# Performance work log

Measured on AMD Instinct MI355X. Metric: run time of the kernel, lower is better.

## Reference

```python
import jax, jax.numpy as jnp
import numpy as np
from jax import lax

Q = 16384      # num questions (hyperedges)
S = 16384      # num students (nodes)
F = 64         # feat_dim
EMB = 64       # emb_dim
H = 32         # student_hist_max
C = 16384      # student_attn_chunk_size
E = 393216     # incidence edges per channel (24 chunks)


def setup_inputs() -> dict:
    key = jax.random.key(0)
    ks = jax.random.split(key, 24)
    rn = lambda k, sh, s=1.0: jax.random.normal(k, sh, dtype=jnp.float32) * s
    ri = lambda k, sh, hi: jax.random.randint(k, sh, 0, hi, dtype=jnp.int32)
    return {
        'x': rn(ks[0], (Q, F)),
        's_emb': rn(ks[1], (S, F)),
        'W_Q': rn(ks[2], (2 * F, F), 0.05), 'b_Q': jnp.zeros((F,), jnp.float32),
        'W_K': rn(ks[3], (F, F), 0.05),     'b_K': jnp.zeros((F,), jnp.float32),
        'W_V': rn(ks[4], (F, F), 0.05),     'b_V': jnp.zeros((F,), jnp.float32),
        'W_fuse': rn(ks[5], (2 * F, F), 0.05), 'b_fuse': jnp.zeros((F,), jnp.float32),
        'W_K2': rn(ks[6], (F, F), 0.05),    'b_K2': jnp.zeros((F,), jnp.float32),
        'W_V2': rn(ks[7], (F, F), 0.05),    'b_V2': jnp.zeros((F,), jnp.float32),
        'W_proj': rn(ks[8], (2 * F, EMB), 0.05), 'b_proj': jnp.zeros((EMB,), jnp.float32),
        'h1_bias': jnp.zeros((2, F), jnp.float32),  # nn.init.zeros_ in source
        'h2_bias': jnp.zeros((2, F), jnp.float32),
        'hist_qid_pos': ri(ks[9], (S, H), Q),
        'hist_cnt_pos': ri(ks[10], (S,), H + 1),
        'hist_qid_neg': ri(ks[11], (S, H), Q),
        'hist_cnt_neg': ri(ks[12], (S,), H + 1),
        'edge_sid_pos': ri(ks[13], (E,), S),
        'edge_qid_pos': ri(ks[14], (E,), Q),
        'edge_sid_neg': ri(ks[15], (E,), S),
        'edge_qid_neg': ri(ks[16], (E,), Q),
    }


def reference(x, s_emb, W_Q, b_Q, W_K, b_K, W_V, b_V, W_fuse, b_fuse,
              W_K2, b_K2, W_V2, b_V2, W_proj, b_proj, h1_bias, h2_bias,
              hist_qid_pos, hist_cnt_pos, hist_qid_neg, hist_cnt_neg,
              edge_sid_pos, edge_qid_pos, edge_sid_neg, edge_qid_neg):
    scale = jnp.float32(1.0 / np.sqrt(F))
    NEG = jnp.float32(-1e9)

    def channel(hist_qid, hist_cnt, e_sid, e_qid, ch):
        # dense per-student history keys/values: [S, H, F]
        xh = x[hist_qid]
        Kh = xh @ W_K + b_K + h1_bias[ch]
        Vh = xh @ W_V + b_V
        mask = jnp.arange(H, dtype=jnp.int32)[None, :] < hist_cnt[:, None]  # [S,H]

        def chunk_fn(args):
            sid, qid = args  # [C]
            # edge-level query: W_Q([x_q || e_u])
            q = jnp.concatenate([x[qid], s_emb[sid]], axis=-1) @ W_Q + b_Q  # [C,F]
            sc = jnp.einsum('cf,chf->ch', q, Kh[sid]) * scale               # [C,H]
            m = mask[sid]
            a = jax.nn.softmax(jnp.where(m, sc, NEG), axis=-1)
            a = jnp.where(m, a, 0.0)  # empty history -> zero output
            return jnp.einsum('ch,chf->cf', a, Vh[sid])                     # [C,F]

        nchunks = E // C
        agg = lax.map(chunk_fn, (e_sid.reshape(nchunks, C), e_qid.reshape(nchunks, C)))
        agg = agg.reshape(E, F)
        # fuse student embedding with history-aggregated context
        s_repr = jnp.concatenate([s_emb[e_sid], agg], axis=-1) @ W_fuse + b_fuse  # [E,F]
        # hop 2: question attends over its member students (segment softmax over e_qid)
        k2 = s_repr @ W_K2 + b_K2 + h2_bias[ch]
        v2 = s_repr @ W_V2 + b_V2
        sc2 = jnp.sum(x[e_qid] * k2, axis=-1) * scale                      # [E]
        mx = jax.ops.segment_max(sc2, e_qid, num_segments=Q)
        ex = jnp.exp(sc2 - mx[e_qid])
        den = jax.ops.segment_sum(ex, e_qid, num_segments=Q)
        alpha = ex / jnp.maximum(den[e_qid], 1e-9)
        return jax.ops.segment_sum(alpha[:, None] * v2, e_qid, num_segments=Q)  # [Q,F]

    pos = channel(hist_qid_pos, hist_cnt_pos, edge_sid_pos, edge_qid_pos, 0)
    neg = channel(hist_qid_neg, hist_cnt_neg, edge_sid_neg, edge_qid_neg, 1)
    return jnp.concatenate([pos, neg], axis=-1) @ W_proj + b_proj  # [Q, EMB]
```

## Files before the change

### kernel.cpp

```cpp
#include <hip/hip_runtime.h>

typedef float v2f __attribute__((ext_vector_type(2)));
typedef float v4f __attribute__((ext_vector_type(4)));

#define QN 16384
#define SN 16384
#define HN 32
#define EN 393216
#define KPAD 68

__global__ __launch_bounds__(256) void prep_kernel(
    const float* __restrict__ x, const float* __restrict__ s_emb,
    const float* __restrict__ W_Q, const float* __restrict__ b_Q,
    const float* __restrict__ W_K, const float* __restrict__ b_K,
    const float* __restrict__ W_V, const float* __restrict__ b_V,
    const float* __restrict__ W_fuse, const float* __restrict__ b_fuse,
    const float* __restrict__ W_K2, const float* __restrict__ b_K2,
    const float* __restrict__ h1b, const float* __restrict__ h2b,
    const int* __restrict__ es_pos, const int* __restrict__ es_neg,
    float* __restrict__ xKpos, float* __restrict__ xKneg,
    float* __restrict__ xVfp, float* __restrict__ xQ1, float* __restrict__ xq2p,
    float* __restrict__ c2pos, float* __restrict__ c2neg,
    float* __restrict__ sQ, float* __restrict__ sfp,
    int* __restrict__ cnt_pos, int* __restrict__ cnt_neg)
{
  __shared__ float xs[512];
  __shared__ float vs[512];
  __shared__ float wk2t[64 * 66];
  const int bid = blockIdx.x;
  const int t = threadIdx.x;
  const int j = t & 31, r = t >> 5;

  if (bid < 2048) {
    const int q = bid * 8 + r;
    if (t < 128) *(v4f*)&xs[t * 4] = *(const v4f*)&x[bid * 512 + t * 4];
    for (int i = 0; i < 16; i++) {
      int idx = i * 256 + t;
      wk2t[(idx & 63) * 66 + (idx >> 6)] = W_K2[idx];
    }
    __syncthreads();

    v2f accK = *(const v2f*)&b_K[2 * j];
    v2f accV = *(const v2f*)&b_V[2 * j];
    v2f accQ = {0.f, 0.f};
    float a2x = 0.f, a2y = 0.f;
    for (int g = 0; g < 64; g++) {
      float xv = xs[r * 64 + g];
      accK += xv * *(const v2f*)&W_K[g * 64 + 2 * j];
      accV += xv * *(const v2f*)&W_V[g * 64 + 2 * j];
      accQ += xv * *(const v2f*)&W_Q[g * 64 + 2 * j];
      a2x += xv * wk2t[g * 66 + j];
      a2y += xv * wk2t[g * 66 + j + 32];
    }
    *(v2f*)&xKpos[q * 64 + 2 * j] = accK + *(const v2f*)&h1b[2 * j];
    *(v2f*)&xKneg[q * 64 + 2 * j] = accK + *(const v2f*)&h1b[64 + 2 * j];
    *(v2f*)&xQ1[q * 64 + 2 * j] = accQ;
    v2f a2 = {a2x, a2y};
    *(v2f*)&xq2p[q * 64 + 2 * j] = a2;
    *(v2f*)&vs[r * 64 + 2 * j] = accV;

    v2f xv2 = *(const v2f*)&xs[r * 64 + 2 * j];
    v2f bb0 = *(const v2f*)&b_K2[2 * j] + *(const v2f*)&h2b[2 * j];
    v2f bb1 = *(const v2f*)&b_K2[2 * j] + *(const v2f*)&h2b[64 + 2 * j];
    v2f t0 = xv2 * bb0, t1 = xv2 * bb1;
    float p0 = t0.x + t0.y, p1v = t1.x + t1.y;
    for (int k = 16; k >= 1; k >>= 1) {
      p0 += __shfl_xor(p0, k, 32);
      p1v += __shfl_xor(p1v, k, 32);
    }
    if (j == 0) { c2pos[q] = p0 * 0.125f; c2neg[q] = p1v * 0.125f; }

    __syncthreads();
    float vfx = 0.f, vfy = 0.f;
    for (int g = 0; g < 64; g++) {
      float vv = vs[r * 64 + g];
      vfx += vv * W_fuse[(64 + g) * 64 + j];
      vfy += vv * W_fuse[(64 + g) * 64 + j + 32];
    }
    v2f vf = {vfx, vfy};
    *(v2f*)&xVfp[q * 64 + 2 * j] = vf;
  } else if (bid < 4096) {
    const int b2 = bid - 2048;
    const int s = b2 * 8 + r;
    if (t < 128) *(v4f*)&xs[t * 4] = *(const v4f*)&s_emb[b2 * 512 + t * 4];
    __syncthreads();
    v2f aq = *(const v2f*)&b_Q[2 * j];
    float afx = b_fuse[j], afy = b_fuse[j + 32];
    for (int g = 0; g < 64; g++) {
      float v = xs[r * 64 + g];
      aq += v * *(const v2f*)&W_Q[(64 + g) * 64 + 2 * j];
      afx += v * W_fuse[g * 64 + j];
      afy += v * W_fuse[g * 64 + j + 32];
    }
    *(v2f*)&sQ[s * 64 + 2 * j] = aq;
    v2f af = {afx, afy};
    *(v2f*)&sfp[s * 64 + 2 * j] = af;
  } else {
    const int hb = bid - 4096;
    const bool neg = hb >= 1536;
    const int* __restrict__ sid = neg ? es_neg : es_pos;
    int* __restrict__ cnt = neg ? cnt_neg : cnt_pos;
    const int i = (neg ? hb - 1536 : hb) * 256 + t;
    atomicAdd(&cnt[sid[i]], 1);
  }
}

__global__ __launch_bounds__(256) void scan_kernel(
    const int* __restrict__ cnt_pos, int* __restrict__ beg_pos, int* __restrict__ cur_pos,
    const int* __restrict__ cnt_neg, int* __restrict__ beg_neg, int* __restrict__ cur_neg) {
  const int* cnt = blockIdx.y ? cnt_neg : cnt_pos;
  int* beg = blockIdx.y ? beg_neg : beg_pos;
  int* cur = blockIdx.y ? cur_neg : cur_pos;
  __shared__ int part[256];
  int t = threadIdx.x;
  int s = 0;
  for (int i = 0; i < 64; i++) s += cnt[i * 256 + t];
  part[t] = s;
  __syncthreads();
  for (int off = 1; off < 256; off <<= 1) {
    int v = (t >= off) ? part[t - off] : 0;
    __syncthreads();
    part[t] += v;
    __syncthreads();
  }
  int run = part[t] - s;
  for (int i = 0; i < 64; i++) {
    int id = i * 256 + t;
    int c = cnt[id];
    beg[id] = run; cur[id] = run;
    run += c;
  }
}

__global__ __launch_bounds__(256) void scatter_kernel(
    const int* __restrict__ sid_pos, const int* __restrict__ qid_pos,
    int* __restrict__ cur_pos, int* __restrict__ csr_pos,
    const int* __restrict__ sid_neg, const int* __restrict__ qid_neg,
    int* __restrict__ cur_neg, int* __restrict__ csr_neg, int n) {
  const int* sid = blockIdx.y ? sid_neg : sid_pos;
  const int* qid = blockIdx.y ? qid_neg : qid_pos;
  int* cursor = blockIdx.y ? cur_neg : cur_pos;
  int* csr_qid = blockIdx.y ? csr_neg : csr_pos;
  int i = blockIdx.x * 256 + threadIdx.x;
  if (i < n) {
    int p = atomicAdd(&cursor[sid[i]], 1);
    csr_qid[p] = qid[i];
  }
}

#define LDBATCH(BASE, Q0,Q1,Q2,Q3, A0,A1,A2,A3, X0,X1,X2,X3, C0,C1,C2,C3) do { \
    int _m = ne - 1; \
    Q0 = csr[ebeg + (BASE)]; \
    Q1 = csr[ebeg + min((BASE) + 1, _m)]; \
    Q2 = csr[ebeg + min((BASE) + 2, _m)]; \
    Q3 = csr[ebeg + min((BASE) + 3, _m)]; \
    A0 = *(const v2f*)&xQ1[(size_t)Q0 * 64 + 2 * c] + sqv; \
    A1 = *(const v2f*)&xQ1[(size_t)Q1 * 64 + 2 * c] + sqv; \
    A2 = *(const v2f*)&xQ1[(size_t)Q2 * 64 + 2 * c] + sqv; \
    A3 = *(const v2f*)&xQ1[(size_t)Q3 * 64 + 2 * c] + sqv; \
    X0 = *(const v2f*)&xq2p[(size_t)Q0 * 64 + 2 * c]; \
    X1 = *(const v2f*)&xq2p[(size_t)Q1 * 64 + 2 * c]; \
    X2 = *(const v2f*)&xq2p[(size_t)Q2 * 64 + 2 * c]; \
    X3 = *(const v2f*)&xq2p[(size_t)Q3 * 64 + 2 * c]; \
    C0 = c2[Q0]; C1 = c2[Q1]; C2 = c2[Q2]; C3 = c2[Q3]; \
  } while (0)

__global__ __launch_bounds__(256, 5) void main_kernel(
    const float* __restrict__ xKpos, const float* __restrict__ xKneg,
    const float* __restrict__ xVfp, const float* __restrict__ xQ1,
    const float* __restrict__ xq2p,
    const float* __restrict__ c2pos, const float* __restrict__ c2neg,
    const float* __restrict__ sQ, const float* __restrict__ sfp,
    const int* __restrict__ hq_pos, const int* __restrict__ hc_pos,
    const int* __restrict__ hq_neg, const int* __restrict__ hc_neg,
    const int* __restrict__ beg_pos, const int* __restrict__ cntS_pos,
    const int* __restrict__ csr_pos,
    const int* __restrict__ beg_neg, const int* __restrict__ cntS_neg,
    const int* __restrict__ csr_neg,
    float* __restrict__ num_pos, float* __restrict__ den_pos,
    float* __restrict__ num_neg, float* __restrict__ den_neg)
{
  const int s = blockIdx.x;
  const int ch = blockIdx.y;
  const float* __restrict__ xK = ch ? xKneg : xKpos;
  const float* __restrict__ c2 = ch ? c2neg : c2pos;
  const int* __restrict__ hq = ch ? hq_neg : hq_pos;
  const int* __restrict__ hc = ch ? hc_neg : hc_pos;
  const int* __restrict__ beg = ch ? beg_neg : beg_pos;
  const int* __restrict__ cntS = ch ? cntS_neg : cntS_pos;
  const int* __restrict__ csr = ch ? csr_neg : csr_pos;
  float* __restrict__ num = ch ? num_neg : num_pos;
  float* __restrict__ den = ch ? den_neg : den_pos;

  const int t = threadIdx.x;
  __shared__ float Kl[HN * KPAD];
  __shared__ float Vl[HN * 64];
  __shared__ float Qg[8 * 4 * 64];
  __shared__ float Al[8 * 32 * 4];
  __shared__ int hql[HN];

  const int hcnt = hc[s];
  if (t < HN) hql[t] = hq[s * HN + t];
  __syncthreads();
  for (int i = 0; i < 2; i++) {
    int idx = i * 256 + t;
    int h = idx >> 4, jj = idx & 15;
    int row = hql[h];
    *(v4f*)&Kl[h * KPAD + jj * 4] = *(const v4f*)&xK[(size_t)row * 64 + jj * 4];
    *(v4f*)&Vl[h * 64 + jj * 4] = *(const v4f*)&xVfp[(size_t)row * 64 + jj * 4];
  }
  const int ebeg = beg[s];
  const int ne = cntS[s];
  __syncthreads();

  const float scale = 0.125f;
  const int g = t >> 5;
  const int c = t & 31;
  float* __restrict__ Qb = &Qg[g * 256];
  float* __restrict__ Ab = &Al[g * 128];
  const v4f* kp = (const v4f*)&Kl[c * KPAD];
  const v2f sqv = *(const v2f*)&sQ[(size_t)s * 64 + 2 * c];
  const v2f sfv = *(const v2f*)&sfp[(size_t)s * 64 + 2 * c];

  int i0 = g * 4;
  if (i0 < ne) {
    int q0, q1, q2, q3;
    v2f a0, a1, a2, a3, x20, x21, x22, x23;
    float cc0, cc1, cc2, cc3;
    LDBATCH(i0, q0, q1, q2, q3, a0, a1, a2, a3, x20, x21, x22, x23, cc0, cc1, cc2, cc3);

    for (; i0 < ne; i0 += 32) {
      const int nb = ne - i0;
      *(v2f*)&Qb[2 * c] = a0;
      *(v2f*)&Qb[64 + 2 * c] = a1;
      *(v2f*)&Qb[128 + 2 * c] = a2;
      *(v2f*)&Qb[192 + 2 * c] = a3;

      int n0, n1, n2, n3;
      v2f na0, na1, na2, na3, nx0, nx1, nx2, nx3;
      float nc0, nc1, nc2, nc3;
      const bool more = (i0 + 32) < ne;
      if (more) {
        LDBATCH(i0 + 32, n0, n1, n2, n3, na0, na1, na2, na3,
                nx0, nx1, nx2, nx3, nc0, nc1, nc2, nc3);
      }

      float s0 = 0.f, s1 = 0.f, s2 = 0.f, s3 = 0.f;
#pragma unroll 4
      for (int k = 0; k < 16; k++) {
        v4f k4 = kp[k];
        v4f qa = ((const v4f*)&Qb[0])[k];
        s0 += qa.x * k4.x + qa.y * k4.y + qa.z * k4.z + qa.w * k4.w;
        v4f qb = ((const v4f*)&Qb[64])[k];
        s1 += qb.x * k4.x + qb.y * k4.y + qb.z * k4.z + qb.w * k4.w;
        v4f qc = ((const v4f*)&Qb[128])[k];
        s2 += qc.x * k4.x + qc.y * k4.y + qc.z * k4.z + qc.w * k4.w;
        v4f qd = ((const v4f*)&Qb[192])[k];
        s3 += qd.x * k4.x + qd.y * k4.y + qd.z * k4.z + qd.w * k4.w;
      }
      const bool valid = (c < hcnt);
      float e0 = valid ? __expf(s0 * scale) : 0.f;
      float e1 = valid ? __expf(s1 * scale) : 0.f;
      float e2 = valid ? __expf(s2 * scale) : 0.f;
      float e3 = valid ? __expf(s3 * scale) : 0.f;
      float d0 = e0, d1 = e1, d2 = e2, d3 = e3;
      for (int k = 16; k >= 1; k >>= 1) {
        d0 += __shfl_xor(d0, k, 32);
        d1 += __shfl_xor(d1, k, 32);
        d2 += __shfl_xor(d2, k, 32);
        d3 += __shfl_xor(d3, k, 32);
      }
      v4f av;
      av.x = (d0 > 0.f) ? e0 / d0 : 0.f;
      av.y = (d1 > 0.f) ? e1 / d1 : 0.f;
      av.z = (d2 > 0.f) ? e2 / d2 : 0.f;
      av.w = (d3 > 0.f) ? e3 / d3 : 0.f;
      *(v4f*)&Ab[c * 4] = av;

      v2f r0 = sfv, r1 = sfv, r2 = sfv, r3 = sfv;
#pragma unroll 8
      for (int h = 0; h < HN; h++) {
        v2f vv = *(const v2f*)&Vl[h * 64 + 2 * c];
        v4f a4 = *(const v4f*)&Ab[h * 4];
        r0 += a4.x * vv;
        r1 += a4.y * vv;
        r2 += a4.z * vv;
        r3 += a4.w * vv;
      }

      {
        float p = r0.x * x20.x + r0.y * x20.y;
        for (int k = 16; k >= 1; k >>= 1) p += __shfl_xor(p, k, 32);
        float ew = __expf(p * scale + cc0);
        atomicAdd(&num[(size_t)q0 * 64 + c], ew * r0.x);
        atomicAdd(&num[(size_t)q0 * 64 + 32 + c], ew * r0.y);
        if (c == 0) atomicAdd(&den[q0], ew);
      }
      if (nb > 1) {
        float p = r1.x * x21.x + r1.y * x21.y;
        for (int k = 16; k >= 1; k >>= 1) p += __shfl_xor(p, k, 32);
        float ew = __expf(p * scale + cc1);
        atomicAdd(&num[(size_t)q1 * 64 + c], ew * r1.x);
        atomicAdd(&num[(size_t)q1 * 64 + 32 + c], ew * r1.y);
        if (c == 0) atomicAdd(&den[q1], ew);
      }
      if (nb > 2) {
        float p = r2.x * x22.x + r2.y * x22.y;
        for (int k = 16; k >= 1; k >>= 1) p += __shfl_xor(p, k, 32);
        float ew = __expf(p * scale + cc2);
        atomicAdd(&num[(size_t)q2 * 64 + c], ew * r2.x);
        atomicAdd(&num[(size_t)q2 * 64 + 32 + c], ew * r2.y);
        if (c == 0) atomicAdd(&den[q2], ew);
      }
      if (nb > 3) {
        float p = r3.x * x23.x + r3.y * x23.y;
        for (int k = 16; k >= 1; k >>= 1) p += __shfl_xor(p, k, 32);
        float ew = __expf(p * scale + cc3);
        atomicAdd(&num[(size_t)q3 * 64 + c], ew * r3.x);
        atomicAdd(&num[(size_t)q3 * 64 + 32 + c], ew * r3.y);
        if (c == 0) atomicAdd(&den[q3], ew);
      }

      q0 = n0; q1 = n1; q2 = n2; q3 = n3;
      a0 = na0; a1 = na1; a2 = na2; a3 = na3;
      x20 = nx0; x21 = nx1; x22 = nx2; x23 = nx3;
      cc0 = nc0; cc1 = nc1; cc2 = nc2; cc3 = nc3;
    }
  }
}

__global__ __launch_bounds__(256) void final_kernel(
    const float* __restrict__ num_pos, const float* __restrict__ den_pos,
    const float* __restrict__ num_neg, const float* __restrict__ den_neg,
    const float* __restrict__ W_V2, const float* __restrict__ b_V2,
    const float* __restrict__ W_proj, const float* __restrict__ b_proj,
    float* __restrict__ out)
{
  __shared__ float np[8 * 64], nn[8 * 64], hp[8 * 64], hn[8 * 64];
  int t = threadIdx.x;
  int j = t & 31, r = t >> 5;
  int q = blockIdx.x * 8 + r;
  if (t < 128) {
    *(v4f*)&np[t * 4] = *(const v4f*)&num_pos[blockIdx.x * 512 + t * 4];
    *(v4f*)&nn[t * 4] = *(const v4f*)&num_neg[blockIdx.x * 512 + t * 4];
  }
  __syncthreads();
  float dp = den_pos[q], dn = den_neg[q];
  float ip = (dp > 0.f) ? 1.f / dp : 0.f;
  float in_ = (dn > 0.f) ? 1.f / dn : 0.f;
  v2f zero = {0.f, 0.f};
  v2f bv = *(const v2f*)&b_V2[2 * j];
  v2f hpv = (dp > 0.f) ? bv : zero;
  v2f hnv = (dn > 0.f) ? bv : zero;
  for (int f = 0; f < 64; f++) {
    v2f w = *(const v2f*)&W_V2[f * 64 + 2 * j];
    hpv += (np[r * 64 + f] * ip) * w;
    hnv += (nn[r * 64 + f] * in_) * w;
  }
  *(v2f*)&hp[r * 64 + 2 * j] = hpv;
  *(v2f*)&hn[r * 64 + 2 * j] = hnv;
  __syncthreads();
  v2f o = *(const v2f*)&b_proj[2 * j];
  for (int f = 0; f < 64; f++) {
    o += hp[r * 64 + f] * *(const v2f*)&W_proj[f * 64 + 2 * j];
    o += hn[r * 64 + f] * *(const v2f*)&W_proj[(64 + f) * 64 + 2 * j];
  }
  *(v2f*)&out[q * 64 + 2 * j] = o;
}

extern "C" void kernel_launch(void* const* d_in, const int* in_sizes, int n_in,
                              void* d_out, int out_size, void* d_ws, size_t ws_size,
                              hipStream_t stream) {
  const float* x      = (const float*)d_in[0];
  const float* s_emb  = (const float*)d_in[1];
  const float* W_Q    = (const float*)d_in[2];
  const float* b_Q    = (const float*)d_in[3];
  const float* W_K    = (const float*)d_in[4];
  const float* b_K    = (const float*)d_in[5];
  const float* W_V    = (const float*)d_in[6];
  const float* b_V    = (const float*)d_in[7];
  const float* W_fuse = (const float*)d_in[8];
  const float* b_fuse = (const float*)d_in[9];
  const float* W_K2   = (const float*)d_in[10];
  const float* b_K2   = (const float*)d_in[11];
  const float* W_V2   = (const float*)d_in[12];
  const float* b_V2   = (const float*)d_in[13];
  const float* W_proj = (const float*)d_in[14];
  const float* b_proj = (const float*)d_in[15];
  const float* h1b    = (const float*)d_in[16];
  const float* h2b    = (const float*)d_in[17];
  const int* hq_pos   = (const int*)d_in[18];
  const int* hc_pos   = (const int*)d_in[19];
  const int* hq_neg   = (const int*)d_in[20];
  const int* hc_neg   = (const int*)d_in[21];
  const int* es_pos   = (const int*)d_in[22];
  const int* eq_pos   = (const int*)d_in[23];
  const int* es_neg   = (const int*)d_in[24];
  const int* eq_neg   = (const int*)d_in[25];
  float* out = (float*)d_out;

  size_t off = 0;
  char* base = (char*)d_ws;
  auto carve = [&](size_t bytes) -> void* {
    void* p = base + off;
    off += (bytes + 255) & ~(size_t)255;
    return p;
  };
  float* num_pos = (float*)carve((size_t)QN * 64 * 4);
  float* num_neg = (float*)carve((size_t)QN * 64 * 4);
  float* den_pos = (float*)carve((size_t)QN * 4);
  float* den_neg = (float*)carve((size_t)QN * 4);
  int* cnt_pos   = (int*)carve((size_t)SN * 4);
  int* cnt_neg   = (int*)carve((size_t)SN * 4);
  size_t zero_bytes = off;
  float* xKpos = (float*)carve((size_t)QN * 64 * 4);
  float* xKneg = (float*)carve((size_t)QN * 64 * 4);
  float* xVfp  = (float*)carve((size_t)QN * 64 * 4);
  float* xQ1   = (float*)carve((size_t)QN * 64 * 4);
  float* xq2p  = (float*)carve((size_t)QN * 64 * 4);
  float* sQ    = (float*)carve((size_t)SN * 64 * 4);
  float* sfp   = (float*)carve((size_t)SN * 64 * 4);
  float* c2pos = (float*)carve((size_t)QN * 4);
  float* c2neg = (float*)carve((size_t)QN * 4);
  int* beg_pos = (int*)carve((size_t)SN * 4);
  int* beg_neg = (int*)carve((size_t)SN * 4);
  int* cur_pos = (int*)carve((size_t)SN * 4);
  int* cur_neg = (int*)carve((size_t)SN * 4);
  int* csr_pos = (int*)carve((size_t)EN * 4);
  int* csr_neg = (int*)carve((size_t)EN * 4);
  if (off > ws_size) return;

  hipMemsetAsync(d_ws, 0, zero_bytes, stream);

  prep_kernel<<<4096 + 2 * (EN / 256), 256, 0, stream>>>(
      x, s_emb, W_Q, b_Q, W_K, b_K, W_V, b_V, W_fuse, b_fuse, W_K2, b_K2,
      h1b, h2b, es_pos, es_neg,
      xKpos, xKneg, xVfp, xQ1, xq2p, c2pos, c2neg, sQ, sfp,
      cnt_pos, cnt_neg);

  scan_kernel<<<dim3(1, 2), 256, 0, stream>>>(cnt_pos, beg_pos, cur_pos,
                                              cnt_neg, beg_neg, cur_neg);
  scatter_kernel<<<dim3(EN / 256, 2), 256, 0, stream>>>(es_pos, eq_pos, cur_pos, csr_pos,
                                                        es_neg, eq_neg, cur_neg, csr_neg, EN);

  main_kernel<<<dim3(SN, 2), 256, 0, stream>>>(
      xKpos, xKneg, xVfp, xQ1, xq2p, c2pos, c2neg, sQ, sfp,
      hq_pos, hc_pos, hq_neg, hc_neg,
      beg_pos, cnt_pos, csr_pos, beg_neg, cnt_neg, csr_neg,
      num_pos, den_pos, num_neg, den_neg);

  final_kernel<<<QN / 8, 256, 0, stream>>>(num_pos, den_pos, num_neg, den_neg,
                                           W_V2, b_V2, W_proj, b_proj, out);
}
```

Measured before the change: 602.4 us.

## Replace hop-2 atomic scatter with question-sorted edge buffer and segment reduction

```diff
diff --git a/kernel.cpp b/kernel.cpp
--- a/kernel.cpp
+++ b/kernel.cpp
@@ -8,6 +8,7 @@
 #define HN 32
 #define EN 393216
 #define KPAD 68
+#define CAP 64
 
 __global__ __launch_bounds__(256) void prep_kernel(
     const float* __restrict__ x, const float* __restrict__ s_emb,
@@ -17,12 +18,12 @@
     const float* __restrict__ W_fuse, const float* __restrict__ b_fuse,
     const float* __restrict__ W_K2, const float* __restrict__ b_K2,
     const float* __restrict__ h1b, const float* __restrict__ h2b,
-    const int* __restrict__ es_pos, const int* __restrict__ es_neg,
+    const int* __restrict__ eq_pos, const int* __restrict__ eq_neg,
     float* __restrict__ xKpos, float* __restrict__ xKneg,
     float* __restrict__ xVfp, float* __restrict__ xQ1, float* __restrict__ xq2p,
     float* __restrict__ c2pos, float* __restrict__ c2neg,
     float* __restrict__ sQ, float* __restrict__ sfp,
-    int* __restrict__ cnt_pos, int* __restrict__ cnt_neg)
+    int* __restrict__ cntq_pos, int* __restrict__ cntq_neg)
 {
   __shared__ float xs[512];
   __shared__ float vs[512];
@@ -98,19 +99,19 @@
   } else {
     const int hb = bid - 4096;
     const bool neg = hb >= 1536;
-    const int* __restrict__ sid = neg ? es_neg : es_pos;
-    int* __restrict__ cnt = neg ? cnt_neg : cnt_pos;
+    const int* __restrict__ eq = neg ? eq_neg : eq_pos;
+    int* __restrict__ cntq = neg ? cntq_neg : cntq_pos;
     const int i = (neg ? hb - 1536 : hb) * 256 + t;
-    atomicAdd(&cnt[sid[i]], 1);
+    atomicAdd(&cntq[eq[i]], 1);
   }
 }
 
 __global__ __launch_bounds__(256) void scan_kernel(
-    const int* __restrict__ cnt_pos, int* __restrict__ beg_pos, int* __restrict__ cur_pos,
-    const int* __restrict__ cnt_neg, int* __restrict__ beg_neg, int* __restrict__ cur_neg) {
-  const int* cnt = blockIdx.y ? cnt_neg : cnt_pos;
-  int* beg = blockIdx.y ? beg_neg : beg_pos;
-  int* cur = blockIdx.y ? cur_neg : cur_pos;
+    const int* __restrict__ cntq_pos, int* __restrict__ begq_pos, int* __restrict__ curq_pos,
+    const int* __restrict__ cntq_neg, int* __restrict__ begq_neg, int* __restrict__ curq_neg) {
+  const int* cnt = blockIdx.y ? cntq_neg : cntq_pos;
+  int* beg = blockIdx.y ? begq_neg : begq_pos;
+  int* cur = blockIdx.y ? curq_neg : curq_pos;
   __shared__ int part[256];
   int t = threadIdx.x;
   int s = 0;
@@ -132,66 +133,47 @@
   }
 }
 
-__global__ __launch_bounds__(256) void scatter_kernel(
+__global__ __launch_bounds__(256) void scatter2_kernel(
     const int* __restrict__ sid_pos, const int* __restrict__ qid_pos,
-    int* __restrict__ cur_pos, int* __restrict__ csr_pos,
+    int* __restrict__ curq_pos, int* __restrict__ cnts_pos, int2* __restrict__ csr_pos,
     const int* __restrict__ sid_neg, const int* __restrict__ qid_neg,
-    int* __restrict__ cur_neg, int* __restrict__ csr_neg, int n) {
-  const int* sid = blockIdx.y ? sid_neg : sid_pos;
-  const int* qid = blockIdx.y ? qid_neg : qid_pos;
-  int* cursor = blockIdx.y ? cur_neg : cur_pos;
-  int* csr_qid = blockIdx.y ? csr_neg : csr_pos;
+    int* __restrict__ curq_neg, int* __restrict__ cnts_neg, int2* __restrict__ csr_neg) {
+  const bool neg = blockIdx.y;
+  const int* sid = neg ? sid_neg : sid_pos;
+  const int* qid = neg ? qid_neg : qid_pos;
+  int* curq = neg ? curq_neg : curq_pos;
+  int* cnts = neg ? cnts_neg : cnts_pos;
+  int2* csr = neg ? csr_neg : csr_pos;
   int i = blockIdx.x * 256 + threadIdx.x;
-  if (i < n) {
-    int p = atomicAdd(&cursor[sid[i]], 1);
-    csr_qid[p] = qid[i];
-  }
-}
-
-#define LDBATCH(BASE, Q0,Q1,Q2,Q3, A0,A1,A2,A3, X0,X1,X2,X3, C0,C1,C2,C3) do { \
+  int s = sid[i], q = qid[i];
+  int ss = atomicAdd(&cnts[s], 1);
+  if (ss < CAP) {
+    int qs = atomicAdd(&curq[q], 1);
+    csr[s * CAP + ss] = make_int2(q, qs);
+  }
+}
+
+#define LDBATCH(BASE, E0,E1,E2,E3, A0,A1,A2,A3) do { \
     int _m = ne - 1; \
-    Q0 = csr[ebeg + (BASE)]; \
-    Q1 = csr[ebeg + min((BASE) + 1, _m)]; \
-    Q2 = csr[ebeg + min((BASE) + 2, _m)]; \
-    Q3 = csr[ebeg + min((BASE) + 3, _m)]; \
-    A0 = *(const v2f*)&xQ1[(size_t)Q0 * 64 + 2 * c] + sqv; \
-    A1 = *(const v2f*)&xQ1[(size_t)Q1 * 64 + 2 * c] + sqv; \
-    A2 = *(const v2f*)&xQ1[(size_t)Q2 * 64 + 2 * c] + sqv; \
-    A3 = *(const v2f*)&xQ1[(size_t)Q3 * 64 + 2 * c] + sqv; \
-    X0 = *(const v2f*)&xq2p[(size_t)Q0 * 64 + 2 * c]; \
-    X1 = *(const v2f*)&xq2p[(size_t)Q1 * 64 + 2 * c]; \
-    X2 = *(const v2f*)&xq2p[(size_t)Q2 * 64 + 2 * c]; \
-    X3 = *(const v2f*)&xq2p[(size_t)Q3 * 64 + 2 * c]; \
-    C0 = c2[Q0]; C1 = c2[Q1]; C2 = c2[Q2]; C3 = c2[Q3]; \
+    E0 = csr2[ebeg + (BASE)]; \
+    E1 = csr2[ebeg + min((BASE) + 1, _m)]; \
+    E2 = csr2[ebeg + min((BASE) + 2, _m)]; \
+    E3 = csr2[ebeg + min((BASE) + 3, _m)]; \
+    A0 = *(const v2f*)&xQ1[(size_t)E0.x * 64 + 2 * c] + sqv; \
+    A1 = *(const v2f*)&xQ1[(size_t)E1.x * 64 + 2 * c] + sqv; \
+    A2 = *(const v2f*)&xQ1[(size_t)E2.x * 64 + 2 * c] + sqv; \
+    A3 = *(const v2f*)&xQ1[(size_t)E3.x * 64 + 2 * c] + sqv; \
   } while (0)
 
 __global__ __launch_bounds__(256, 5) void main_kernel(
-    const float* __restrict__ xKpos, const float* __restrict__ xKneg,
-    const float* __restrict__ xVfp, const float* __restrict__ xQ1,
-    const float* __restrict__ xq2p,
-    const float* __restrict__ c2pos, const float* __restrict__ c2neg,
+    const float* __restrict__ xK, const float* __restrict__ xVfp,
+    const float* __restrict__ xQ1,
     const float* __restrict__ sQ, const float* __restrict__ sfp,
-    const int* __restrict__ hq_pos, const int* __restrict__ hc_pos,
-    const int* __restrict__ hq_neg, const int* __restrict__ hc_neg,
-    const int* __restrict__ beg_pos, const int* __restrict__ cntS_pos,
-    const int* __restrict__ csr_pos,
-    const int* __restrict__ beg_neg, const int* __restrict__ cntS_neg,
-    const int* __restrict__ csr_neg,
-    float* __restrict__ num_pos, float* __restrict__ den_pos,
-    float* __restrict__ num_neg, float* __restrict__ den_neg)
+    const int* __restrict__ hq, const int* __restrict__ hc,
+    const int* __restrict__ cnts, const int2* __restrict__ csr2,
+    float* __restrict__ rbuf)
 {
   const int s = blockIdx.x;
-  const int ch = blockIdx.y;
-  const float* __restrict__ xK = ch ? xKneg : xKpos;
-  const float* __restrict__ c2 = ch ? c2neg : c2pos;
-  const int* __restrict__ hq = ch ? hq_neg : hq_pos;
-  const int* __restrict__ hc = ch ? hc_neg : hc_pos;
-  const int* __restrict__ beg = ch ? beg_neg : beg_pos;
-  const int* __restrict__ cntS = ch ? cntS_neg : cntS_pos;
-  const int* __restrict__ csr = ch ? csr_neg : csr_pos;
-  float* __restrict__ num = ch ? num_neg : num_pos;
-  float* __restrict__ den = ch ? den_neg : den_pos;
-
   const int t = threadIdx.x;
   __shared__ float Kl[HN * KPAD];
   __shared__ float Vl[HN * 64];
@@ -209,8 +191,8 @@
     *(v4f*)&Kl[h * KPAD + jj * 4] = *(const v4f*)&xK[(size_t)row * 64 + jj * 4];
     *(v4f*)&Vl[h * 64 + jj * 4] = *(const v4f*)&xVfp[(size_t)row * 64 + jj * 4];
   }
-  const int ebeg = beg[s];
-  const int ne = cntS[s];
+  const int ebeg = s * CAP;
+  const int ne = min(cnts[s], CAP);
   __syncthreads();
 
   const float scale = 0.125f;
@@ -224,10 +206,9 @@
 
   int i0 = g * 4;
   if (i0 < ne) {
-    int q0, q1, q2, q3;
-    v2f a0, a1, a2, a3, x20, x21, x22, x23;
-    float cc0, cc1, cc2, cc3;
-    LDBATCH(i0, q0, q1, q2, q3, a0, a1, a2, a3, x20, x21, x22, x23, cc0, cc1, cc2, cc3);
+    int2 e0, e1, e2, e3;
+    v2f a0, a1, a2, a3;
+    LDBATCH(i0, e0, e1, e2, e3, a0, a1, a2, a3);
 
     for (; i0 < ne; i0 += 32) {
       const int nb = ne - i0;
@@ -236,14 +217,10 @@
       *(v2f*)&Qb[128 + 2 * c] = a2;
       *(v2f*)&Qb[192 + 2 * c] = a3;
 
-      int n0, n1, n2, n3;
-      v2f na0, na1, na2, na3, nx0, nx1, nx2, nx3;
-      float nc0, nc1, nc2, nc3;
+      int2 f0, f1, f2, f3;
+      v2f na0, na1, na2, na3;
       const bool more = (i0 + 32) < ne;
-      if (more) {
-        LDBATCH(i0 + 32, n0, n1, n2, n3, na0, na1, na2, na3,
-                nx0, nx1, nx2, nx3, nc0, nc1, nc2, nc3);
-      }
+      if (more) LDBATCH(i0 + 32, f0, f1, f2, f3, na0, na1, na2, na3);
 
       float s0 = 0.f, s1 = 0.f, s2 = 0.f, s3 = 0.f;
 #pragma unroll 4
@@ -259,11 +236,11 @@
         s3 += qd.x * k4.x + qd.y * k4.y + qd.z * k4.z + qd.w * k4.w;
       }
       const bool valid = (c < hcnt);
-      float e0 = valid ? __expf(s0 * scale) : 0.f;
-      float e1 = valid ? __expf(s1 * scale) : 0.f;
-      float e2 = valid ? __expf(s2 * scale) : 0.f;
-      float e3 = valid ? __expf(s3 * scale) : 0.f;
-      float d0 = e0, d1 = e1, d2 = e2, d3 = e3;
+      float e0w = valid ? __expf(s0 * scale) : 0.f;
+      float e1w = valid ? __expf(s1 * scale) : 0.f;
+      float e2w = valid ? __expf(s2 * scale) : 0.f;
+      float e3w = valid ? __expf(s3 * scale) : 0.f;
+      float d0 = e0w, d1 = e1w, d2 = e2w, d3 = e3w;
       for (int k = 16; k >= 1; k >>= 1) {
         d0 += __shfl_xor(d0, k, 32);
         d1 += __shfl_xor(d1, k, 32);
@@ -271,10 +248,10 @@
         d3 += __shfl_xor(d3, k, 32);
       }
       v4f av;
-      av.x = (d0 > 0.f) ? e0 / d0 : 0.f;
-      av.y = (d1 > 0.f) ? e1 / d1 : 0.f;
-      av.z = (d2 > 0.f) ? e2 / d2 : 0.f;
-      av.w = (d3 > 0.f) ? e3 / d3 : 0.f;
+      av.x = (d0 > 0.f) ? e0w / d0 : 0.f;
+      av.y = (d1 > 0.f) ? e1w / d1 : 0.f;
+      av.z = (d2 > 0.f) ? e2w / d2 : 0.f;
+      av.w = (d3 > 0.f) ? e3w / d3 : 0.f;
       *(v4f*)&Ab[c * 4] = av;
 
       v2f r0 = sfv, r1 = sfv, r2 = sfv, r3 = sfv;
@@ -288,84 +265,79 @@
         r3 += a4.w * vv;
       }
 
-      {
-        float p = r0.x * x20.x + r0.y * x20.y;
-        for (int k = 16; k >= 1; k >>= 1) p += __shfl_xor(p, k, 32);
-        float ew = __expf(p * scale + cc0);
-        atomicAdd(&num[(size_t)q0 * 64 + c], ew * r0.x);
-        atomicAdd(&num[(size_t)q0 * 64 + 32 + c], ew * r0.y);
-        if (c == 0) atomicAdd(&den[q0], ew);
-      }
-      if (nb > 1) {
-        float p = r1.x * x21.x + r1.y * x21.y;
-        for (int k = 16; k >= 1; k >>= 1) p += __shfl_xor(p, k, 32);
-        float ew = __expf(p * scale + cc1);
-        atomicAdd(&num[(size_t)q1 * 64 + c], ew * r1.x);
-        atomicAdd(&num[(size_t)q1 * 64 + 32 + c], ew * r1.y);
-        if (c == 0) atomicAdd(&den[q1], ew);
-      }
-      if (nb > 2) {
-        float p = r2.x * x22.x + r2.y * x22.y;
-        for (int k = 16; k >= 1; k >>= 1) p += __shfl_xor(p, k, 32);
-        float ew = __expf(p * scale + cc2);
-        atomicAdd(&num[(size_t)q2 * 64 + c], ew * r2.x);
-        atomicAdd(&num[(size_t)q2 * 64 + 32 + c], ew * r2.y);
-        if (c == 0) atomicAdd(&den[q2], ew);
-      }
-      if (nb > 3) {
-        float p = r3.x * x23.x + r3.y * x23.y;
-        for (int k = 16; k >= 1; k >>= 1) p += __shfl_xor(p, k, 32);
-        float ew = __expf(p * scale + cc3);
-        atomicAdd(&num[(size_t)q3 * 64 + c], ew * r3.x);
-        atomicAdd(&num[(size_t)q3 * 64 + 32 + c], ew * r3.y);
-        if (c == 0) atomicAdd(&den[q3], ew);
-      }
-
-      q0 = n0; q1 = n1; q2 = n2; q3 = n3;
+      *(v2f*)&rbuf[(size_t)e0.y * 64 + 2 * c] = r0;
+      if (nb > 1) *(v2f*)&rbuf[(size_t)e1.y * 64 + 2 * c] = r1;
+      if (nb > 2) *(v2f*)&rbuf[(size_t)e2.y * 64 + 2 * c] = r2;
+      if (nb > 3) *(v2f*)&rbuf[(size_t)e3.y * 64 + 2 * c] = r3;
+
+      e0 = f0; e1 = f1; e2 = f2; e3 = f3;
       a0 = na0; a1 = na1; a2 = na2; a3 = na3;
-      x20 = nx0; x21 = nx1; x22 = nx2; x23 = nx3;
-      cc0 = nc0; cc1 = nc1; cc2 = nc2; cc3 = nc3;
-    }
-  }
-}
-
-__global__ __launch_bounds__(256) void final_kernel(
-    const float* __restrict__ num_pos, const float* __restrict__ den_pos,
-    const float* __restrict__ num_neg, const float* __restrict__ den_neg,
+    }
+  }
+}
+
+__global__ __launch_bounds__(256) void hop2_kernel(
+    const float* __restrict__ rbuf,
+    const int* __restrict__ begq, const int* __restrict__ curq,
+    const float* __restrict__ xq2p, const float* __restrict__ c2,
     const float* __restrict__ W_V2, const float* __restrict__ b_V2,
+    float* __restrict__ hout,
+    int do_proj, const float* __restrict__ hpos,
     const float* __restrict__ W_proj, const float* __restrict__ b_proj,
     float* __restrict__ out)
 {
-  __shared__ float np[8 * 64], nn[8 * 64], hp[8 * 64], hn[8 * 64];
-  int t = threadIdx.x;
-  int j = t & 31, r = t >> 5;
-  int q = blockIdx.x * 8 + r;
-  if (t < 128) {
-    *(v4f*)&np[t * 4] = *(const v4f*)&num_pos[blockIdx.x * 512 + t * 4];
-    *(v4f*)&nn[t * 4] = *(const v4f*)&num_neg[blockIdx.x * 512 + t * 4];
-  }
-  __syncthreads();
-  float dp = den_pos[q], dn = den_neg[q];
-  float ip = (dp > 0.f) ? 1.f / dp : 0.f;
-  float in_ = (dn > 0.f) ? 1.f / dn : 0.f;
-  v2f zero = {0.f, 0.f};
-  v2f bv = *(const v2f*)&b_V2[2 * j];
-  v2f hpv = (dp > 0.f) ? bv : zero;
-  v2f hnv = (dn > 0.f) ? bv : zero;
+  __shared__ float ls[8][64];
+  __shared__ float lp[8][64];
+  const int t = threadIdx.x;
+  const int g = t >> 5, c = t & 31;
+  const int q = blockIdx.x * 8 + g;
+  const float scale = 0.125f;
+
+  const int beg = begq[q];
+  const int ne = curq[q] - beg;
+  const v2f x2 = *(const v2f*)&xq2p[(size_t)q * 64 + 2 * c];
+  const float cc = c2[q];
+
+  v2f num = {0.f, 0.f};
+  float den = 0.f;
+  const float* rp = rbuf + (size_t)beg * 64 + 2 * c;
+  for (int e = 0; e < ne; e++) {
+    v2f r = *(const v2f*)(rp + (size_t)e * 64);
+    float p = r.x * x2.x + r.y * x2.y;
+    for (int k = 16; k >= 1; k >>= 1) p += __shfl_xor(p, k, 32);
+    float ew = __expf(p * scale + cc);
+    den += ew;
+    num += ew * r;
+  }
+  float inv = (den > 0.f) ? 1.f / den : 0.f;
+  v2f rb = num * inv;
+  ls[g][c] = rb.x;
+  ls[g][c + 32] = rb.y;
+
+  float hx = (den > 0.f) ? b_V2[c] : 0.f;
+  float hy = (den > 0.f) ? b_V2[c + 32] : 0.f;
   for (int f = 0; f < 64; f++) {
-    v2f w = *(const v2f*)&W_V2[f * 64 + 2 * j];
-    hpv += (np[r * 64 + f] * ip) * w;
-    hnv += (nn[r * 64 + f] * in_) * w;
-  }
-  *(v2f*)&hp[r * 64 + 2 * j] = hpv;
-  *(v2f*)&hn[r * 64 + 2 * j] = hnv;
-  __syncthreads();
-  v2f o = *(const v2f*)&b_proj[2 * j];
-  for (int f = 0; f < 64; f++) {
-    o += hp[r * 64 + f] * *(const v2f*)&W_proj[f * 64 + 2 * j];
-    o += hn[r * 64 + f] * *(const v2f*)&W_proj[(64 + f) * 64 + 2 * j];
-  }
-  *(v2f*)&out[q * 64 + 2 * j] = o;
+    float rv = ls[g][f];
+    hx += rv * W_V2[f * 64 + c];
+    hy += rv * W_V2[f * 64 + c + 32];
+  }
+  hout[(size_t)q * 64 + c] = hx;
+  hout[(size_t)q * 64 + c + 32] = hy;
+
+  if (do_proj) {
+    lp[g][c] = hpos[(size_t)q * 64 + c];
+    lp[g][c + 32] = hpos[(size_t)q * 64 + c + 32];
+    ls[g][c] = hx;
+    ls[g][c + 32] = hy;
+    float ox = b_proj[c], oy = b_proj[c + 32];
+    for (int f = 0; f < 64; f++) {
+      float hpv = lp[g][f], hnv = ls[g][f];
+      ox += hpv * W_proj[f * 64 + c] + hnv * W_proj[(64 + f) * 64 + c];
+      oy += hpv * W_proj[f * 64 + c + 32] + hnv * W_proj[(64 + f) * 64 + c + 32];
+    }
+    out[(size_t)q * 64 + c] = ox;
+    out[(size_t)q * 64 + c + 32] = oy;
+  }
 }
 
 extern "C" void kernel_launch(void* const* d_in, const int* in_sizes, int n_in,
@@ -406,12 +378,10 @@
     off += (bytes + 255) & ~(size_t)255;
     return p;
   };
-  float* num_pos = (float*)carve((size_t)QN * 64 * 4);
-  float* num_neg = (float*)carve((size_t)QN * 64 * 4);
-  float* den_pos = (float*)carve((size_t)QN * 4);
-  float* den_neg = (float*)carve((size_t)QN * 4);
-  int* cnt_pos   = (int*)carve((size_t)SN * 4);
-  int* cnt_neg   = (int*)carve((size_t)SN * 4);
+  int* cnts_pos = (int*)carve((size_t)SN * 4);
+  int* cnts_neg = (int*)carve((size_t)SN * 4);
+  int* cntq_pos = (int*)carve((size_t)QN * 4);
+  int* cntq_neg = (int*)carve((size_t)QN * 4);
   size_t zero_bytes = off;
   float* xKpos = (float*)carve((size_t)QN * 64 * 4);
   float* xKneg = (float*)carve((size_t)QN * 64 * 4);
@@ -422,33 +392,41 @@
   float* sfp   = (float*)carve((size_t)SN * 64 * 4);
   float* c2pos = (float*)carve((size_t)QN * 4);
   float* c2neg = (float*)carve((size_t)QN * 4);
-  int* beg_pos = (int*)carve((size_t)SN * 4);
-  int* beg_neg = (int*)carve((size_t)SN * 4);
-  int* cur_pos = (int*)carve((size_t)SN * 4);
-  int* cur_neg = (int*)carve((size_t)SN * 4);
-  int* csr_pos = (int*)carve((size_t)EN * 4);
-  int* csr_neg = (int*)carve((size_t)EN * 4);
+  int* begq_pos = (int*)carve((size_t)QN * 4);
+  int* begq_neg = (int*)carve((size_t)QN * 4);
+  int* curq_pos = (int*)carve((size_t)QN * 4);
+  int* curq_neg = (int*)carve((size_t)QN * 4);
+  int2* csr_pos = (int2*)carve((size_t)SN * CAP * 8);
+  int2* csr_neg = (int2*)carve((size_t)SN * CAP * 8);
+  float* rbuf   = (float*)carve((size_t)EN * 64 * 4);
+  float* hposb  = (float*)carve((size_t)QN * 64 * 4);
+  float* hnegb  = (float*)carve((size_t)QN * 64 * 4);
   if (off > ws_size) return;
 
   hipMemsetAsync(d_ws, 0, zero_bytes, stream);
 
   prep_kernel<<<4096 + 2 * (EN / 256), 256, 0, stream>>>(
       x, s_emb, W_Q, b_Q, W_K, b_K, W_V, b_V, W_fuse, b_fuse, W_K2, b_K2,
-      h1b, h2b, es_pos, es_neg,
+      h1b, h2b, eq_pos, eq_neg,
       xKpos, xKneg, xVfp, xQ1, xq2p, c2pos, c2neg, sQ, sfp,
-      cnt_pos, cnt_neg);
-
-  scan_kernel<<<dim3(1, 2), 256, 0, stream>>>(cnt_pos, beg_pos, cur_pos,
-                                              cnt_neg, beg_neg, cur_neg);
-  scatter_kernel<<<dim3(EN / 256, 2), 256, 0, stream>>>(es_pos, eq_pos, cur_pos, csr_pos,
-                                                        es_neg, eq_neg, cur_neg, csr_neg, EN);
-
-  main_kernel<<<dim3(SN, 2), 256, 0, stream>>>(
-      xKpos, xKneg, xVfp, xQ1, xq2p, c2pos, c2neg, sQ, sfp,
-      hq_pos, hc_pos, hq_neg, hc_neg,
-      beg_pos, cnt_pos, csr_pos, beg_neg, cnt_neg, csr_neg,
-      num_pos, den_pos, num_neg, den_neg);
-
-  final_kernel<<<QN / 8, 256, 0, stream>>>(num_pos, den_pos, num_neg, den_neg,
-                                           W_V2, b_V2, W_proj, b_proj, out);
-}
+      cntq_pos, cntq_neg);
+
+  scan_kernel<<<dim3(1, 2), 256, 0, stream>>>(cntq_pos, begq_pos, curq_pos,
+                                              cntq_neg, begq_neg, curq_neg);
+
+  scatter2_kernel<<<dim3(EN / 256, 2), 256, 0, stream>>>(
+      es_pos, eq_pos, curq_pos, cnts_pos, csr_pos,
+      es_neg, eq_neg, curq_neg, cnts_neg, csr_neg);
+
+  main_kernel<<<SN, 256, 0, stream>>>(xKpos, xVfp, xQ1, sQ, sfp,
+                                      hq_pos, hc_pos, cnts_pos, csr_pos, rbuf);
+  hop2_kernel<<<QN / 8, 256, 0, stream>>>(rbuf, begq_pos, curq_pos, xq2p, c2pos,
+                                          W_V2, b_V2, hposb,
+                                          0, hposb, W_proj, b_proj, out);
+
+  main_kernel<<<SN, 256, 0, stream>>>(xKneg, xVfp, xQ1, sQ, sfp,
+                                      hq_neg, hc_neg, cnts_neg, csr_neg, rbuf);
+  hop2_kernel<<<QN / 8, 256, 0, stream>>>(rbuf, begq_neg, curq_neg, xq2p, c2neg,
+                                          W_V2, b_V2, hnegb,
+                                          1, hposb, W_proj, b_proj, out);
+}
```

Measured after the change: 598.9 us. About the same (-0.6%).
